# Optimization experiments

Measured on AMD Instinct MI355X. Metric: run time of the kernel, lower is better.

The kernel has to match this reference:

```python
import jax, jax.numpy as jnp
import numpy as np

N_EMBD = 1024
D_FF = 4 * N_EMBD
RANK = 4
NUM_LOOPS = 4
SCALE = 1.0 / RANK  # alpha=1.0 / r=4


def setup_inputs() -> dict:
    key = jax.random.key(0)
    ks = jax.random.split(key, 8)
    B, T = 8, 2048
    x = jax.random.normal(ks[0], (B, T, N_EMBD), dtype=jnp.float32)
    # base linears (torch nn.Linear weight layout: [out, in]), bias=False
    W1 = jax.random.normal(ks[1], (D_FF, N_EMBD), dtype=jnp.float32) * (1.0 / np.sqrt(N_EMBD))
    W2 = jax.random.normal(ks[2], (N_EMBD, D_FF), dtype=jnp.float32) * (1.0 / np.sqrt(D_FF))
    # LoRA factors: A [num_loops, r, in], B [num_loops, out, r]
    # (torch inits lora_B to zeros; we use small random values so the LoRA path is exercised)
    A1 = jax.random.normal(ks[3], (NUM_LOOPS, RANK, N_EMBD), dtype=jnp.float32) * (1.0 / np.sqrt(N_EMBD))
    B1 = jax.random.normal(ks[4], (NUM_LOOPS, D_FF, RANK), dtype=jnp.float32) * 0.01
    A2 = jax.random.normal(ks[5], (NUM_LOOPS, RANK, D_FF), dtype=jnp.float32) * (1.0 / np.sqrt(D_FF))
    B2 = jax.random.normal(ks[6], (NUM_LOOPS, N_EMBD, RANK), dtype=jnp.float32) * 0.01
    adapter_id = 1
    return {"x": x, "W1": W1, "A1": A1, "B1": B1, "W2": W2, "A2": A2, "B2": B2,
            "adapter_id": adapter_id}


def _lora_linear(x, W, A, B, adapter_id):
    # base: x @ W.T  (torch F.linear)
    out = jnp.einsum('btd,fd->btf', x, W)
    Aa = A[adapter_id]  # [r, in]
    Ba = B[adapter_id]  # [out, r]
    # low-rank correction: ((x @ A.T) @ B.T) * scale
    delta = jnp.einsum('btr,fr->btf', jnp.einsum('btd,rd->btr', x, Aa), Ba) * SCALE
    return out + delta


def reference(x, W1, A1, B1, W2, A2, B2, adapter_id):
    h = jax.nn.relu(_lora_linear(x, W1, A1, B1, adapter_id))
    out = _lora_linear(h, W2, A2, B2, adapter_id)
    # Dropout in eval mode (identity); see notes.
    return out
```

## Files before the change

### kernel.cpp

```cpp
#include <hip/hip_runtime.h>
#include <stdint.h>

typedef __bf16 bf16;
typedef __attribute__((ext_vector_type(8))) __bf16 bf16x8;
typedef __attribute__((ext_vector_type(4))) float f32x4;

#define LORA_SCALE 0.25f

__device__ __forceinline__ void gload_lds16(const bf16* g, bf16* l) {
    __builtin_amdgcn_global_load_lds(
        (const __attribute__((address_space(1))) uint32_t*)g,
        (__attribute__((address_space(3))) uint32_t*)l,
        16, 0, 0);
}

__device__ __forceinline__ bf16x8 cvt8(const float* p) {
    f32x4 a = *(const f32x4*)p;
    f32x4 b = *(const f32x4*)(p + 4);
    bf16x8 r;
    r[0] = (bf16)a[0]; r[1] = (bf16)a[1]; r[2] = (bf16)a[2]; r[3] = (bf16)a[3];
    r[4] = (bf16)b[0]; r[5] = (bf16)b[1]; r[6] = (bf16)b[2]; r[7] = (bf16)b[3];
    return r;
}

__global__ __launch_bounds__(256)
void cvt_weights(const float* __restrict__ in1, bf16* __restrict__ out1, int n1,
                 const float* __restrict__ in2, bf16* __restrict__ out2, int n2) {
    const int64_t idx = (int64_t)(blockIdx.x * 256 + threadIdx.x) * 8;
    if (idx < n1) *(bf16x8*)&out1[idx] = cvt8(&in1[idx]);
    else          *(bf16x8*)&out2[idx - n1] = cvt8(&in2[idx - n1]);
}

__global__ __launch_bounds__(256)
void lora1(const float* __restrict__ X, const float* __restrict__ Aall,
           const int* __restrict__ adapter, float* __restrict__ T,
           bf16* __restrict__ Xb)
{
    const int K = 1024;
    const int gid = blockIdx.x * 256 + threadIdx.x;
    const int aid = adapter[0];
    const float* Aa = Aall + (int64_t)aid * 4 * K;
    const int wid  = gid >> 6;
    const int lane = threadIdx.x & 63;
    const int m0   = wid * 4;

    float acc[4][4];
    #pragma unroll
    for (int rr = 0; rr < 4; rr++)
        #pragma unroll
        for (int r = 0; r < 4; r++) acc[rr][r] = 0.f;

    #pragma unroll
    for (int it = 0; it < K / 512; it++) {
        const int k = it * 512 + lane * 8;
        float av[4][8];
        #pragma unroll
        for (int r = 0; r < 4; r++) {
            f32x4 a = *(const f32x4*)&Aa[r * K + k];
            f32x4 b = *(const f32x4*)&Aa[r * K + k + 4];
            av[r][0]=a[0]; av[r][1]=a[1]; av[r][2]=a[2]; av[r][3]=a[3];
            av[r][4]=b[0]; av[r][5]=b[1]; av[r][6]=b[2]; av[r][7]=b[3];
        }
        #pragma unroll
        for (int rr = 0; rr < 4; rr++) {
            const float* xp = X + (int64_t)(m0 + rr) * K + k;
            f32x4 a = *(const f32x4*)xp;
            f32x4 b = *(const f32x4*)(xp + 4);
            float xv[8] = {a[0],a[1],a[2],a[3],b[0],b[1],b[2],b[3]};
            bf16x8 xb;
            #pragma unroll
            for (int e = 0; e < 8; e++) xb[e] = (bf16)xv[e];
            *(bf16x8*)&Xb[(int64_t)(m0 + rr) * K + k] = xb;
            #pragma unroll
            for (int r = 0; r < 4; r++)
                #pragma unroll
                for (int e = 0; e < 8; e++)
                    acc[rr][r] += xv[e] * av[r][e];
        }
    }
    #pragma unroll
    for (int rr = 0; rr < 4; rr++)
        #pragma unroll
        for (int r = 0; r < 4; r++)
            #pragma unroll
            for (int off = 32; off >= 1; off >>= 1)
                acc[rr][r] += __shfl_xor(acc[rr][r], off);
    if (lane == 0) {
        #pragma unroll
        for (int rr = 0; rr < 4; rr++) {
            f32x4 t;
            t[0] = acc[rr][0]; t[1] = acc[rr][1]; t[2] = acc[rr][2]; t[3] = acc[rr][3];
            *(f32x4*)&T[(int64_t)(m0 + rr) * 4] = t;
        }
    }
}

__global__ __launch_bounds__(256)
void t2_reduce(const float* __restrict__ T2p, float* __restrict__ T2,
               int M, int NP) {
    const int i = blockIdx.x * 256 + threadIdx.x;
    float s = 0.f;
    for (int p = 0; p < NP; p++) s += T2p[(int64_t)p * M * 4 + i];
    T2[i] = s;
}

template<bool RELU, typename CT, int PART, bool FUSET2>
__global__ __launch_bounds__(512, 2)
void gemm_lora8(const bf16* __restrict__ A,
                const bf16* __restrict__ Bm,
                CT* __restrict__ C,
                const float* __restrict__ Tlo,
                const float* __restrict__ Blo,
                const int* __restrict__ adapter,
                const float* __restrict__ A2,
                float* __restrict__ T2p,
                int M, int N, int K)
{
    __shared__ alignas(16) bf16 smem[65536];

    const int tid  = threadIdx.x;
    const int lane = tid & 63;
    const int w    = tid >> 6;
    const int quad = lane >> 4;
    const int l16  = lane & 15;

    int bx, by;
    {
        const int Nt = gridDim.x, Mt = gridDim.y;
        const int id = blockIdx.y * Nt + blockIdx.x;
        const int xcd = id & 7, k = id >> 3;
        if (PART == 0) { const int q = Nt >> 3; bx = xcd * q + (k % q); by = k / q; }
        else           { const int q = Mt >> 3; bx = k % Nt; by = xcd * q + (k / Nt); }
    }
    const int nBase = bx * 256;
    const int mBase = by * 256;
    const int wm = (w >> 1) * 64;
    const int wn = (w & 1) * 128;

    f32x4 acc[4][8];
    #pragma unroll
    for (int i = 0; i < 4; i++)
        #pragma unroll
        for (int j = 0; j < 8; j++)
            #pragma unroll
            for (int e = 0; e < 4; e++) acc[i][j][e] = 0.f;

    const bf16* gA = A  + (int64_t)mBase * K;
    const bf16* gB = Bm + (int64_t)nBase * K;

    const int sq    = (tid & 3) ^ ((tid >> 3) & 3);
    const int srow  = ((tid >> 3) << 1) | ((tid >> 2) & 1);
    const bf16* sA0 = gA + (int64_t)srow * K + sq * 8;
    const bf16* sA1 = gA + (int64_t)(srow + 128) * K + sq * 8;
    const bf16* sB0 = gB + (int64_t)srow * K + sq * 8;
    const bf16* sB1 = gB + (int64_t)(srow + 128) * K + sq * 8;
    const int dstW  = w * 512;

    const int pc8  = (quad ^ ((l16 >> 1) & 3)) * 8;
    const int aOff = (wm + l16) * 32 + pc8;
    const int bOff = (wn + l16) * 32 + pc8;

    const int NT = K >> 6;

    auto stage = [&](const bf16* s0, const bf16* s1, int t, int uidx) {
        bf16* u = smem + ((t & 1) * 4 + uidx) * 8192;
        const int co = t * 64 + (uidx >> 1) * 32;
        gload_lds16(s0 + co, u + dstW);
        gload_lds16(s1 + co, u + dstW + 4096);
    };

    stage(sA0, sA1, 0, 0); stage(sB0, sB1, 0, 1);
    stage(sA0, sA1, 0, 2); stage(sB0, sB1, 0, 3);
    if (NT > 1) {
        asm volatile("s_waitcnt vmcnt(4)" ::: "memory");
        stage(sA0, sA1, 1, 0); stage(sB0, sB1, 1, 1); stage(sA0, sA1, 1, 2);
        asm volatile("s_waitcnt vmcnt(6)" ::: "memory");
    } else {
        asm volatile("s_waitcnt vmcnt(0)" ::: "memory");
    }
    __builtin_amdgcn_s_barrier();
    __builtin_amdgcn_sched_barrier(0);

    for (int t = 0; t < NT; ++t) {
        const bf16* u0 = smem + (t & 1) * 32768;
        const bf16* u1 = u0 + 8192;
        const bf16* u2 = u0 + 16384;
        const bf16* u3 = u0 + 24576;
        const bool sNext  = (t + 1 < NT);
        const bool sNext2 = (t + 2 < NT);

        bf16x8 a0[4], bA[4];
        #pragma unroll
        for (int mi = 0; mi < 4; mi++) a0[mi] = *(const bf16x8*)&u0[aOff + mi * 512];
        #pragma unroll
        for (int j = 0; j < 4; j++)   bA[j]  = *(const bf16x8*)&u1[bOff + j * 512];
        if (sNext) stage(sB0, sB1, t + 1, 3);
        __builtin_amdgcn_s_barrier();
        __builtin_amdgcn_sched_barrier(0);
        asm volatile("s_waitcnt lgkmcnt(0)" ::: "memory");
        __builtin_amdgcn_s_setprio(1);
        #pragma unroll
        for (int mi = 0; mi < 4; mi++)
            #pragma unroll
            for (int j = 0; j < 4; j++)
                acc[mi][j] = __builtin_amdgcn_mfma_f32_16x16x32_bf16(a0[mi], bA[j], acc[mi][j], 0, 0, 0);
        __builtin_amdgcn_s_setprio(0);
        __builtin_amdgcn_s_barrier();
        __builtin_amdgcn_sched_barrier(0);

        bf16x8 bB[4];
        #pragma unroll
        for (int j = 0; j < 4; j++) bB[j] = *(const bf16x8*)&u1[bOff + (4 + j) * 512];
        if (sNext2) stage(sA0, sA1, t + 2, 0);
        __builtin_amdgcn_s_barrier();
        __builtin_amdgcn_sched_barrier(0);
        asm volatile("s_waitcnt lgkmcnt(0)" ::: "memory");
        __builtin_amdgcn_s_setprio(1);
        #pragma unroll
        for (int mi = 0; mi < 4; mi++)
            #pragma unroll
            for (int j = 0; j < 4; j++)
                acc[mi][4 + j] = __builtin_amdgcn_mfma_f32_16x16x32_bf16(a0[mi], bB[j], acc[mi][4 + j], 0, 0, 0);
        __builtin_amdgcn_s_setprio(0);
        __builtin_amdgcn_s_barrier();
        __builtin_amdgcn_sched_barrier(0);

        bf16x8 a1[4], bC[4];
        #pragma unroll
        for (int mi = 0; mi < 4; mi++) a1[mi] = *(const bf16x8*)&u2[aOff + mi * 512];
        #pragma unroll
        for (int j = 0; j < 4; j++)   bC[j]  = *(const bf16x8*)&u3[bOff + j * 512];
        if (sNext2) stage(sB0, sB1, t + 2, 1);
        __builtin_amdgcn_s_barrier();
        __builtin_amdgcn_sched_barrier(0);
        asm volatile("s_waitcnt lgkmcnt(0)" ::: "memory");
        __builtin_amdgcn_s_setprio(1);
        #pragma unroll
        for (int mi = 0; mi < 4; mi++)
            #pragma unroll
            for (int j = 0; j < 4; j++)
                acc[mi][j] = __builtin_amdgcn_mfma_f32_16x16x32_bf16(a1[mi], bC[j], acc[mi][j], 0, 0, 0);
        __builtin_amdgcn_s_setprio(0);
        __builtin_amdgcn_s_barrier();
        __builtin_amdgcn_sched_barrier(0);

        bf16x8 bD[4];
        #pragma unroll
        for (int j = 0; j < 4; j++) bD[j] = *(const bf16x8*)&u3[bOff + (4 + j) * 512];
        if (sNext2) stage(sA0, sA1, t + 2, 2);
        __builtin_amdgcn_s_barrier();
        __builtin_amdgcn_sched_barrier(0);
        asm volatile("s_waitcnt lgkmcnt(0)" ::: "memory");
        __builtin_amdgcn_s_setprio(1);
        #pragma unroll
        for (int mi = 0; mi < 4; mi++)
            #pragma unroll
            for (int j = 0; j < 4; j++)
                acc[mi][4 + j] = __builtin_amdgcn_mfma_f32_16x16x32_bf16(a1[mi], bD[j], acc[mi][4 + j], 0, 0, 0);
        __builtin_amdgcn_s_setprio(0);
        if (sNext) {
            if (sNext2) asm volatile("s_waitcnt vmcnt(6)" ::: "memory");
            else        asm volatile("s_waitcnt vmcnt(0)" ::: "memory");
        }
        __builtin_amdgcn_s_barrier();
        __builtin_amdgcn_sched_barrier(0);
    }

    const int aid = adapter[0];
    const float* Ba = Blo + (int64_t)aid * N * 4;

    f32x4 bv[8];
    #pragma unroll
    for (int j = 0; j < 8; j++) {
        const int f = nBase + wn + j * 16 + l16;
        bv[j] = *(const f32x4*)&Ba[(int64_t)f * 4];
    }

    float a2v[8][4];
    if constexpr (FUSET2) {
        const float* A2a = A2 + (int64_t)aid * 4 * N;
        #pragma unroll
        for (int j = 0; j < 8; j++) {
            const int f = nBase + wn + j * 16 + l16;
            #pragma unroll
            for (int r2 = 0; r2 < 4; r2++)
                a2v[j][r2] = A2a[(int64_t)r2 * N + f];
        }
    }
    float* T2row = FUSET2 ? T2p + (int64_t)(bx * 2 + (w & 1)) * M * 4 : nullptr;

    if constexpr (sizeof(CT) == 2) {
        bf16* scratch = smem + w * (16 * 136);
        #pragma unroll
        for (int mi = 0; mi < 4; mi++) {
            f32x4 tv[4];
            #pragma unroll
            for (int r = 0; r < 4; r++) {
                const int m = mBase + wm + mi * 16 + quad * 4 + r;
                tv[r] = *(const f32x4*)&Tlo[(int64_t)m * 4];
            }
            float tp[4][4];
            if constexpr (FUSET2)
                #pragma unroll
                for (int r = 0; r < 4; r++)
                    #pragma unroll
                    for (int r2 = 0; r2 < 4; r2++) tp[r][r2] = 0.f;
            #pragma unroll
            for (int j = 0; j < 8; j++) {
                #pragma unroll
                for (int r = 0; r < 4; r++) {
                    const float d = tv[r][0] * bv[j][0] + tv[r][1] * bv[j][1]
                                  + tv[r][2] * bv[j][2] + tv[r][3] * bv[j][3];
                    float v = acc[mi][j][r] + LORA_SCALE * d;
                    if (RELU) v = v > 0.f ? v : 0.f;
                    if constexpr (FUSET2)
                        #pragma unroll
                        for (int r2 = 0; r2 < 4; r2++) tp[r][r2] += v * a2v[j][r2];
                    scratch[(quad * 4 + r) * 136 + j * 16 + l16] = (bf16)v;
                }
            }
            if constexpr (FUSET2) {
                #pragma unroll
                for (int r = 0; r < 4; r++)
                    #pragma unroll
                    for (int r2 = 0; r2 < 4; r2++)
                        #pragma unroll
                        for (int off = 8; off >= 1; off >>= 1)
                            tp[r][r2] += __shfl_xor(tp[r][r2], off);
                if (l16 == 0) {
                    #pragma unroll
                    for (int r = 0; r < 4; r++) {
                        const int m = mBase + wm + mi * 16 + quad * 4 + r;
                        f32x4 o;
                        o[0] = tp[r][0]; o[1] = tp[r][1];
                        o[2] = tp[r][2]; o[3] = tp[r][3];
                        *(f32x4*)&T2row[(int64_t)m * 4] = o;
                    }
                }
            }
            #pragma unroll
            for (int it = 0; it < 4; it++) {
                const int cid = it * 64 + lane;
                const int row = cid >> 4, c8 = cid & 15;
                bf16x8 vv = *(const bf16x8*)&scratch[row * 136 + c8 * 8];
                const int m = mBase + wm + mi * 16 + row;
                *(bf16x8*)&C[(int64_t)m * N + nBase + wn + c8 * 8] = vv;
            }
        }
    } else {
        float* scratchf = (float*)smem + w * (16 * 132);
        #pragma unroll
        for (int mi = 0; mi < 4; mi++) {
            f32x4 tv[4];
            #pragma unroll
            for (int r = 0; r < 4; r++) {
                const int m = mBase + wm + mi * 16 + quad * 4 + r;
                tv[r] = *(const f32x4*)&Tlo[(int64_t)m * 4];
            }
            #pragma unroll
            for (int j = 0; j < 8; j++) {
                #pragma unroll
                for (int r = 0; r < 4; r++) {
                    const float d = tv[r][0] * bv[j][0] + tv[r][1] * bv[j][1]
                                  + tv[r][2] * bv[j][2] + tv[r][3] * bv[j][3];
                    float v = acc[mi][j][r] + LORA_SCALE * d;
                    if (RELU) v = v > 0.f ? v : 0.f;
                    scratchf[(quad * 4 + r) * 132 + j * 16 + l16] = v;
                }
            }
            #pragma unroll
            for (int it = 0; it < 8; it++) {
                const int cid = it * 64 + lane;
                const int row = cid >> 5, c4 = cid & 31;
                f32x4 vv = *(const f32x4*)&scratchf[row * 132 + c4 * 4];
                const int m = mBase + wm + mi * 16 + row;
                *(f32x4*)&C[(int64_t)m * N + nBase + wn + c4 * 4] = vv;
            }
        }
    }
}

extern "C" void kernel_launch(void* const* d_in, const int* in_sizes, int n_in,
                              void* d_out, int out_size, void* d_ws, size_t ws_size,
                              hipStream_t stream) {
    const float* x  = (const float*)d_in[0];
    const float* W1 = (const float*)d_in[1];
    const float* A1 = (const float*)d_in[2];
    const float* B1 = (const float*)d_in[3];
    const float* W2 = (const float*)d_in[4];
    const float* A2 = (const float*)d_in[5];
    const float* B2 = (const float*)d_in[6];
    const int* adapter = (const int*)d_in[7];
    float* out = (float*)d_out;

    const int M = 16384, D = 1024, F = 4096;
    const int Nt1 = F / 256;

    bf16*  h   = (bf16*)d_ws;
    bf16*  xb  = h + (size_t)M * F;
    bf16*  wb1 = xb + (size_t)M * D;
    bf16*  wb2 = wb1 + (size_t)F * D;
    float* t1  = (float*)(wb2 + (size_t)D * F);
    float* t2  = t1 + (size_t)M * 4;
    float* t2p = t2 + (size_t)M * 4;

    lora1<<<M / 16, 256, 0, stream>>>(x, A1, adapter, t1, xb);
    cvt_weights<<<(2 * F * D) / 2048, 256, 0, stream>>>(W1, wb1, F * D, W2, wb2, D * F);
    dim3 g1(F / 256, M / 256);
    gemm_lora8<true, bf16, 0, true><<<g1, 512, 0, stream>>>(
        xb, wb1, h, t1, B1, adapter, A2, t2p, M, F, D);
    t2_reduce<<<(M * 4) / 256, 256, 0, stream>>>(t2p, t2, M, 2 * Nt1);
    dim3 g2(D / 256, M / 256);
    gemm_lora8<false, float, 1, false><<<g2, 512, 0, stream>>>(
        h, wb2, out, t2, B2, adapter, nullptr, nullptr, M, D, F);
}
```

Baseline: 449.5 us.

## Software-pipeline LDS fragment reads one phase ahead of MFMA in GEMM main loop

Restructures the GEMM inner loop so the LDS reads for the next MFMA phase are issued before the current phase's MFMAs run, with register double buffering (aX/aY, bX/bY). The next tile's first fragments are prefetched at the end of each iteration. This removes one barrier per phase and moves the global-load waitcnt earlier. The goal is to hide LDS read latency behind matrix math. In exchange it needs more VGPRs, which could pressure the 2-blocks-per-CU occupancy, and the barrier/waitcnt placement becomes more delicate.

Measured after the change: 430.7 us. 1.04x faster.

```diff
diff --git a/kernel.cpp b/kernel.cpp
--- a/kernel.cpp
+++ b/kernel.cpp
@@ -104,9 +104,19 @@
     T2[i] = s;
 }
 
+#define MFMA16(AF, BF, JOFF)                                                     \
+    __builtin_amdgcn_s_setprio(1);                                              \
+    _Pragma("unroll")                                                            \
+    for (int mi = 0; mi < 4; mi++)                                               \
+        _Pragma("unroll")                                                        \
+        for (int j = 0; j < 4; j++)                                              \
+            acc[mi][JOFF + j] = __builtin_amdgcn_mfma_f32_16x16x32_bf16(         \
+                AF[mi], BF[j], acc[mi][JOFF + j], 0, 0, 0);                      \
+    __builtin_amdgcn_s_setprio(0);
+
 template<bool RELU, typename CT, int PART, bool FUSET2>
 __global__ __launch_bounds__(512, 2)
-void gemm_lora8(const bf16* __restrict__ A,
+void gemm_lora9(const bf16* __restrict__ A,
                 const bf16* __restrict__ Bm,
                 CT* __restrict__ C,
                 const float* __restrict__ Tlo,
@@ -172,7 +182,6 @@
     stage(sA0, sA1, 0, 0); stage(sB0, sB1, 0, 1);
     stage(sA0, sA1, 0, 2); stage(sB0, sB1, 0, 3);
     if (NT > 1) {
-        asm volatile("s_waitcnt vmcnt(4)" ::: "memory");
         stage(sA0, sA1, 1, 0); stage(sB0, sB1, 1, 1); stage(sA0, sA1, 1, 2);
         asm volatile("s_waitcnt vmcnt(6)" ::: "memory");
     } else {
@@ -181,87 +190,67 @@
     __builtin_amdgcn_s_barrier();
     __builtin_amdgcn_sched_barrier(0);
 
+    bf16x8 aX[4], aY[4], bX[4], bY[4];
+    {
+        const bf16* p0 = smem;
+        const bf16* p1 = smem + 8192;
+        #pragma unroll
+        for (int i = 0; i < 4; i++) aX[i] = *(const bf16x8*)&p0[aOff + i * 512];
+        #pragma unroll
+        for (int j = 0; j < 4; j++) bX[j] = *(const bf16x8*)&p1[bOff + j * 512];
+    }
+
     for (int t = 0; t < NT; ++t) {
-        const bf16* u0 = smem + (t & 1) * 32768;
-        const bf16* u1 = u0 + 8192;
-        const bf16* u2 = u0 + 16384;
-        const bf16* u3 = u0 + 24576;
+        const bf16* ub = smem + (t & 1) * 32768;
+        const bf16* u1 = ub + 8192;
+        const bf16* u2 = ub + 16384;
+        const bf16* u3 = ub + 24576;
+        const bf16* n0 = smem + ((t + 1) & 1) * 32768;
+        const bf16* n1 = n0 + 8192;
         const bool sNext  = (t + 1 < NT);
         const bool sNext2 = (t + 2 < NT);
 
-        bf16x8 a0[4], bA[4];
-        #pragma unroll
-        for (int mi = 0; mi < 4; mi++) a0[mi] = *(const bf16x8*)&u0[aOff + mi * 512];
-        #pragma unroll
-        for (int j = 0; j < 4; j++)   bA[j]  = *(const bf16x8*)&u1[bOff + j * 512];
+        asm volatile("s_waitcnt lgkmcnt(0)" ::: "memory");
+        __builtin_amdgcn_sched_barrier(0);
+        #pragma unroll
+        for (int j = 0; j < 4; j++) bY[j] = *(const bf16x8*)&u1[bOff + (4 + j) * 512];
         if (sNext) stage(sB0, sB1, t + 1, 3);
+        MFMA16(aX, bX, 0)
         __builtin_amdgcn_s_barrier();
         __builtin_amdgcn_sched_barrier(0);
+
         asm volatile("s_waitcnt lgkmcnt(0)" ::: "memory");
-        __builtin_amdgcn_s_setprio(1);
-        #pragma unroll
-        for (int mi = 0; mi < 4; mi++)
-            #pragma unroll
-            for (int j = 0; j < 4; j++)
-                acc[mi][j] = __builtin_amdgcn_mfma_f32_16x16x32_bf16(a0[mi], bA[j], acc[mi][j], 0, 0, 0);
-        __builtin_amdgcn_s_setprio(0);
+        __builtin_amdgcn_sched_barrier(0);
+        #pragma unroll
+        for (int i = 0; i < 4; i++) aY[i] = *(const bf16x8*)&u2[aOff + i * 512];
+        #pragma unroll
+        for (int j = 0; j < 4; j++) bX[j] = *(const bf16x8*)&u3[bOff + j * 512];
+        if (sNext2) stage(sA0, sA1, t + 2, 0);
+        MFMA16(aX, bY, 4)
         __builtin_amdgcn_s_barrier();
         __builtin_amdgcn_sched_barrier(0);
 
-        bf16x8 bB[4];
-        #pragma unroll
-        for (int j = 0; j < 4; j++) bB[j] = *(const bf16x8*)&u1[bOff + (4 + j) * 512];
-        if (sNext2) stage(sA0, sA1, t + 2, 0);
+        asm volatile("s_waitcnt lgkmcnt(0)" ::: "memory");
+        __builtin_amdgcn_sched_barrier(0);
+        #pragma unroll
+        for (int j = 0; j < 4; j++) bY[j] = *(const bf16x8*)&u3[bOff + (4 + j) * 512];
+        if (sNext2) stage(sB0, sB1, t + 2, 1);
+        if (sNext2)      asm volatile("s_waitcnt vmcnt(4)" ::: "memory");
+        else if (sNext)  asm volatile("s_waitcnt vmcnt(0)" ::: "memory");
+        MFMA16(aY, bX, 0)
         __builtin_amdgcn_s_barrier();
         __builtin_amdgcn_sched_barrier(0);
+
         asm volatile("s_waitcnt lgkmcnt(0)" ::: "memory");
-        __builtin_amdgcn_s_setprio(1);
-        #pragma unroll
-        for (int mi = 0; mi < 4; mi++)
-            #pragma unroll
-            for (int j = 0; j < 4; j++)
-                acc[mi][4 + j] = __builtin_amdgcn_mfma_f32_16x16x32_bf16(a0[mi], bB[j], acc[mi][4 + j], 0, 0, 0);
-        __builtin_amdgcn_s_setprio(0);
-        __builtin_amdgcn_s_barrier();
-        __builtin_amdgcn_sched_barrier(0);
-
-        bf16x8 a1[4], bC[4];
-        #pragma unroll
-        for (int mi = 0; mi < 4; mi++) a1[mi] = *(const bf16x8*)&u2[aOff + mi * 512];
-        #pragma unroll
-        for (int j = 0; j < 4; j++)   bC[j]  = *(const bf16x8*)&u3[bOff + j * 512];
-        if (sNext2) stage(sB0, sB1, t + 2, 1);
-        __builtin_amdgcn_s_barrier();
-        __builtin_amdgcn_sched_barrier(0);
-        asm volatile("s_waitcnt lgkmcnt(0)" ::: "memory");
-        __builtin_amdgcn_s_setprio(1);
-        #pragma unroll
-        for (int mi = 0; mi < 4; mi++)
-            #pragma unroll
-            for (int j = 0; j < 4; j++)
-                acc[mi][j] = __builtin_amdgcn_mfma_f32_16x16x32_bf16(a1[mi], bC[j], acc[mi][j], 0, 0, 0);
-        __builtin_amdgcn_s_setprio(0);
-        __builtin_amdgcn_s_barrier();
-        __builtin_amdgcn_sched_barrier(0);
-
-        bf16x8 bD[4];
-        #pragma unroll
-        for (int j = 0; j < 4; j++) bD[j] = *(const bf16x8*)&u3[bOff + (4 + j) * 512];
+        __builtin_amdgcn_sched_barrier(0);
+        if (sNext) {
+            #pragma unroll
+            for (int i = 0; i < 4; i++) aX[i] = *(const bf16x8*)&n0[aOff + i * 512];
+            #pragma unroll
+            for (int j = 0; j < 4; j++) bX[j] = *(const bf16x8*)&n1[bOff + j * 512];
+        }
         if (sNext2) stage(sA0, sA1, t + 2, 2);
-        __builtin_amdgcn_s_barrier();
-        __builtin_amdgcn_sched_barrier(0);
-        asm volatile("s_waitcnt lgkmcnt(0)" ::: "memory");
-        __builtin_amdgcn_s_setprio(1);
-        #pragma unroll
-        for (int mi = 0; mi < 4; mi++)
-            #pragma unroll
-            for (int j = 0; j < 4; j++)
-                acc[mi][4 + j] = __builtin_amdgcn_mfma_f32_16x16x32_bf16(a1[mi], bD[j], acc[mi][4 + j], 0, 0, 0);
-        __builtin_amdgcn_s_setprio(0);
-        if (sNext) {
-            if (sNext2) asm volatile("s_waitcnt vmcnt(6)" ::: "memory");
-            else        asm volatile("s_waitcnt vmcnt(0)" ::: "memory");
-        }
+        MFMA16(aY, bY, 4)
         __builtin_amdgcn_s_barrier();
         __builtin_amdgcn_sched_barrier(0);
     }
@@ -407,10 +396,10 @@
     lora1<<<M / 16, 256, 0, stream>>>(x, A1, adapter, t1, xb);
     cvt_weights<<<(2 * F * D) / 2048, 256, 0, stream>>>(W1, wb1, F * D, W2, wb2, D * F);
     dim3 g1(F / 256, M / 256);
-    gemm_lora8<true, bf16, 0, true><<<g1, 512, 0, stream>>>(
+    gemm_lora9<true, bf16, 0, true><<<g1, 512, 0, stream>>>(
         xb, wb1, h, t1, B1, adapter, A2, t2p, M, F, D);
     t2_reduce<<<(M * 4) / 256, 256, 0, stream>>>(t2p, t2, M, 2 * Nt1);
     dim3 g2(D / 256, M / 256);
-    gemm_lora8<false, float, 1, false><<<g2, 512, 0, stream>>>(
+    gemm_lora9<false, float, 1, false><<<g2, 512, 0, stream>>>(
         h, wb2, out, t2, B2, adapter, nullptr, nullptr, M, D, F);
 }
```
